# Performance work log

Measured on AMD Instinct MI355X. Metric: run time of the kernel, lower is better.

## Reference

```python
import jax, jax.numpy as jnp
import numpy as np

NUM_OBJ_CLS = 9  # len(anchor_scales) * len(anchor_ratios) = 3 * 3


def _bce_with_logits_sum(x, y):
    # Numerically stable BCEWithLogitsLoss(reduction='sum'):
    # max(x,0) - x*y + log(1 + exp(-|x|)), summed over all elements.
    return jnp.sum(jnp.maximum(x, 0.0) - x * y + jnp.log1p(jnp.exp(-jnp.abs(x))))


def setup_inputs() -> dict:
    key = jax.random.key(0)
    k1, k2, k3 = jax.random.split(key, 3)
    B, H, W = 16, 192, 192
    pred = jax.random.normal(k1, (B, 6 * NUM_OBJ_CLS, H, W), dtype=jnp.float32)
    target = jax.random.uniform(k2, (B, 6, H, W), dtype=jnp.float32)
    loc = jax.random.randint(k3, (128, 2), 0, H)  # (x, y) coords into HxW map
    return {"pred": pred, "target": target, "loc": loc}


def reference(pred, target, loc):
    # Objectness loss: for i in range(0, 18, 2):
    #   BCE_sum(pred[:, i], target[:, 0]) + BCE_sum(pred[:, i+1], target[:, 1])
    # then divided by NUM_OBJ_CLS. Even channels pair with target ch 0,
    # odd channels with target ch 1. Vectorized over the 9 anchor classes.
    even = pred[:, 0:2 * NUM_OBJ_CLS:2]   # [B, 9, H, W]
    odd = pred[:, 1:2 * NUM_OBJ_CLS:2]    # [B, 9, H, W]
    t0 = target[:, 0:1]                    # [B, 1, H, W] broadcasts over 9
    t1 = target[:, 1:2]
    loss_obj = (_bce_with_logits_sum(even, t0) + _bce_with_logits_sum(odd, t1))
    loss_obj = loss_obj / NUM_OBJ_CLS
    # NOTE: in the original module the box-loss branch computes pred_box /
    # target_box gathers inside python loops but never accumulates them into
    # loss_box, which stays 0. Faithfully, the output is loss_obj alone; loc
    # does not affect the result.
    return loss_obj
```

## Files before the change

kernel.cpp:

```cpp
#include <hip/hip_runtime.h>
#include <hip/hip_bf16.h>


#define HW_     (192 * 192)
#define HW4_    (HW_ / 4)
#define NCH_    18
#define PREDC_  54
#define TGTC_   6
#define NB_     16

__device__ __forceinline__ float bce_elem(float x, float y) {
    return fmaxf(x, 0.0f) - x * y + log1pf(__expf(-fabsf(x)));
}

__global__ __launch_bounds__(256) void rpn_bce_kernel(
        const float* __restrict__ pred,
        const float* __restrict__ target,
        float* __restrict__ out) {
    const int total = NB_ * NCH_ * HW4_;
    const int stride = gridDim.x * blockDim.x;

    const float4* __restrict__ p4 = (const float4*)pred;
    const float4* __restrict__ t4 = (const float4*)target;

    float acc = 0.0f;
    for (int i = blockIdx.x * blockDim.x + threadIdx.x; i < total; i += stride) {
        int b  = i / (NCH_ * HW4_);
        int r  = i - b * (NCH_ * HW4_);
        int c  = r / HW4_;
        int hw = r - c * HW4_;

        float4 x = p4[(b * PREDC_ + c) * HW4_ + hw];
        float4 y = t4[(b * TGTC_ + (c & 1)) * HW4_ + hw];

        acc += bce_elem(x.x, y.x);
        acc += bce_elem(x.y, y.y);
        acc += bce_elem(x.z, y.z);
        acc += bce_elem(x.w, y.w);
    }

    #pragma unroll
    for (int off = 32; off > 0; off >>= 1)
        acc += __shfl_down(acc, off, 64);

    __shared__ float wsum[4];
    const int lane = threadIdx.x & 63;
    const int wid  = threadIdx.x >> 6;
    if (lane == 0) wsum[wid] = acc;
    __syncthreads();

    if (threadIdx.x == 0) {
        float s = wsum[0] + wsum[1] + wsum[2] + wsum[3];
        atomicAdd(out, s * (1.0f / 9.0f));
    }
}

extern "C" void kernel_launch(void* const* d_in, const int* in_sizes, int n_in,
                              void* d_out, int out_size, void* d_ws, size_t ws_size,
                              hipStream_t stream) {
    const float* pred   = (const float*)d_in[0];
    const float* target = (const float*)d_in[1];
    float* out = (float*)d_out;

    hipMemsetAsync(out, 0, sizeof(float), stream);

    rpn_bce_kernel<<<2048, 256, 0, stream>>>(pred, target, out);
}
```

Measured before the change: 189.5 us.

## Map blocks to planes with unrolled float4 loads and fast log

Replaces the grid-stride loop with a 2D grid where each block row handles one (batch, channel) plane. Each thread processes four float4 elements with unrolled independent loads. This removes the per-iteration integer divisions and raises memory-level parallelism. It also swaps log1pf for __logf(1+exp), which is cheaper but less accurate when the exponential term is tiny.

```diff
diff --git a/kernel.cpp b/kernel.cpp
--- a/kernel.cpp
+++ b/kernel.cpp
@@ -8,31 +8,33 @@
 #define PREDC_  54
 #define TGTC_   6
 #define NB_     16
+#define CHUNKS_ 9
+#define F4_PER_THREAD_ 4
 
 __device__ __forceinline__ float bce_elem(float x, float y) {
-    return fmaxf(x, 0.0f) - x * y + log1pf(__expf(-fabsf(x)));
+    return fmaxf(x, 0.0f) - x * y + __logf(1.0f + __expf(-fabsf(x)));
 }
 
 __global__ __launch_bounds__(256) void rpn_bce_kernel(
         const float* __restrict__ pred,
         const float* __restrict__ target,
         float* __restrict__ out) {
-    const int total = NB_ * NCH_ * HW4_;
-    const int stride = gridDim.x * blockDim.x;
+    const int plane = blockIdx.y;
+    const int b = plane / NCH_;
+    const int c = plane - b * NCH_;
 
-    const float4* __restrict__ p4 = (const float4*)pred;
-    const float4* __restrict__ t4 = (const float4*)target;
+    const float4* __restrict__ p4 = (const float4*)pred   + (size_t)(b * PREDC_ + c) * HW4_;
+    const float4* __restrict__ t4 = (const float4*)target + (size_t)(b * TGTC_ + (c & 1)) * HW4_;
+
+    const int base = blockIdx.x * 256 + threadIdx.x;
+    const int step = CHUNKS_ * 256;
 
     float acc = 0.0f;
-    for (int i = blockIdx.x * blockDim.x + threadIdx.x; i < total; i += stride) {
-        int b  = i / (NCH_ * HW4_);
-        int r  = i - b * (NCH_ * HW4_);
-        int c  = r / HW4_;
-        int hw = r - c * HW4_;
-
-        float4 x = p4[(b * PREDC_ + c) * HW4_ + hw];
-        float4 y = t4[(b * TGTC_ + (c & 1)) * HW4_ + hw];
-
+    #pragma unroll
+    for (int k = 0; k < F4_PER_THREAD_; ++k) {
+        const int idx = base + k * step;
+        float4 x = p4[idx];
+        float4 y = t4[idx];
         acc += bce_elem(x.x, y.x);
         acc += bce_elem(x.y, y.y);
         acc += bce_elem(x.z, y.z);
@@ -64,5 +66,6 @@
 
     hipMemsetAsync(out, 0, sizeof(float), stream);
 
-    rpn_bce_kernel<<<2048, 256, 0, stream>>>(pred, target, out);
+    dim3 grid(CHUNKS_, NB_ * NCH_);
+    rpn_bce_kernel<<<grid, 256, 0, stream>>>(pred, target, out);
 }
```

After: 198.2 us. 1.05x slower.
